# Kernel optimization log

Measured on AMD Instinct MI355X. Metric: run time of the kernel, lower is better.

The kernel has to match this reference:

```python
import jax, jax.numpy as jnp
import numpy as np

DIM = 768
HEADS = 12
HEAD_DIM = DIM // HEADS


def setup_inputs() -> dict:
    key = jax.random.key(0)
    ks = jax.random.split(key, 5)
    B, S = 4, 2048
    init = 0.02
    x = jax.random.normal(ks[0], (B, S, DIM), dtype=jnp.float32)
    w_qkv = jax.random.normal(ks[1], (DIM, 3 * DIM), dtype=jnp.float32) * init
    b_qkv = jnp.zeros((3 * DIM,), dtype=jnp.float32)
    w_out = jax.random.normal(ks[2], (DIM, DIM), dtype=jnp.float32) * init
    b_out = jnp.zeros((DIM,), dtype=jnp.float32)
    return {"x": x, "w_qkv": w_qkv, "b_qkv": b_qkv, "w_out": w_out, "b_out": b_out}


def reference(x, w_qkv, b_qkv, w_out, b_out):
    B, S, D = x.shape
    # QKV projection: [B,S,3D] -> [3,B,H,S,hd]
    qkv = x @ w_qkv + b_qkv
    qkv = qkv.reshape(B, S, 3, HEADS, HEAD_DIM).transpose(2, 0, 3, 1, 4)
    q, k, v = qkv[0], qkv[1], qkv[2]
    # NOTE: original scales by 1/sqrt(head_num), not 1/sqrt(head_dim)
    scale = 1.0 / jnp.sqrt(jnp.float32(HEADS))
    scores = jnp.einsum("bhqd,bhkd->bhqk", q, k) * scale
    attn = jax.nn.softmax(scores, axis=-1)
    out = jnp.einsum("bhqk,bhkd->bhqd", attn, v)
    out = out.transpose(0, 2, 1, 3).reshape(B, S, D)
    return out @ w_out + b_out
```

## Files before the change

### kernel.cpp

```cpp
#include <hip/hip_runtime.h>
#include <hip/hip_bf16.h>
#include <cstdint>
#include <cstddef>

#define HEADS 12
#define HD    64
#define NB    4
#define SEQ   2048
#define DIM   768
#define NQKV  2304

static constexpr float QSCALE = 0.2886751345948129f * 1.4426950408889634f;

typedef __attribute__((ext_vector_type(8))) short short8;
typedef __attribute__((ext_vector_type(4))) short short4v;
typedef __attribute__((ext_vector_type(4))) float f32x4;

__device__ inline unsigned short f2bf(float x) {
    union { float f; uint32_t u; } v; v.f = x;
    return (unsigned short)((v.u + 0x7fffu + ((v.u >> 16) & 1u)) >> 16);
}

__device__ inline unsigned short f2bf_fast(float x) {
    __hip_bfloat16 h = __float2bfloat16(x);
    unsigned short u;
    __builtin_memcpy(&u, &h, 2);
    return u;
}

__device__ inline void gld16(const void* g, void* l) {
    __builtin_amdgcn_global_load_lds(
        (const __attribute__((address_space(1))) unsigned int*)g,
        (__attribute__((address_space(3))) unsigned int*)l, 16, 0, 0);
}

__device__ inline void transpose_tile(
    const float* __restrict__ w, unsigned short* __restrict__ wT,
    int ncols, int nrows, int bx, int by, float (*tile)[65])
{
    const int k0 = by * 64;
    const int n0 = bx * 64;
    const int tr = threadIdx.x >> 4;
    const int tc4 = (threadIdx.x & 15) * 4;
    #pragma unroll
    for (int it = 0; it < 4; ++it) {
        const int kk = tr + it * 16;
        *reinterpret_cast<float4*>(&tile[kk][tc4]) =
            *reinterpret_cast<const float4*>(w + (size_t)(k0 + kk) * ncols + n0 + tc4);
    }
    __syncthreads();
    #pragma unroll
    for (int it = 0; it < 4; ++it) {
        const int nn = tr + it * 16;
        short4v o;
        #pragma unroll
        for (int r = 0; r < 4; ++r) o[r] = (short)f2bf(tile[tc4 + r][nn]);
        *reinterpret_cast<short4v*>(wT + (size_t)(n0 + nn) * nrows + k0 + tc4) = o;
    }
}

__global__ __launch_bounds__(256) void prep_kernel(
    const float* __restrict__ x, unsigned short* __restrict__ xb,
    const float* __restrict__ wq, unsigned short* __restrict__ wqT,
    const float* __restrict__ wo, unsigned short* __restrict__ woT)
{
    __shared__ float tile[64][65];
    const int bid = blockIdx.x;
    if (bid < 3072) {
        const size_t i = ((size_t)bid * 256 + threadIdx.x) * 8;
        const float4 a = *reinterpret_cast<const float4*>(x + i);
        const float4 b = *reinterpret_cast<const float4*>(x + i + 4);
        short8 o;
        o[0] = (short)f2bf(a.x); o[1] = (short)f2bf(a.y);
        o[2] = (short)f2bf(a.z); o[3] = (short)f2bf(a.w);
        o[4] = (short)f2bf(b.x); o[5] = (short)f2bf(b.y);
        o[6] = (short)f2bf(b.z); o[7] = (short)f2bf(b.w);
        *reinterpret_cast<short8*>(xb + i) = o;
    } else if (bid < 3072 + 432) {
        const int r = bid - 3072;
        transpose_tile(wq, wqT, NQKV, DIM, r % 36, r / 36, tile);
    } else {
        const int r = bid - 3504;
        transpose_tile(wo, woT, DIM, DIM, r % 12, r / 12, tile);
    }
}

__global__ __launch_bounds__(512) void qkv_gemm_bf16(
    const unsigned short* __restrict__ A,
    const unsigned short* __restrict__ BT,
    const float* __restrict__ bias,
    unsigned short* __restrict__ qb, unsigned short* __restrict__ kb,
    unsigned short* __restrict__ vt)
{
    __shared__ __align__(16) unsigned short As[2][128][64];
    __shared__ __align__(16) unsigned short Bs[2][128][64];

    const int tid = threadIdx.x;
    const int wave = tid >> 6;
    const int lane = tid & 63;
    const int col = lane & 15;
    const int g = lane >> 4;
    const int m0 = blockIdx.y * 128;
    const int n0 = blockIdx.x * 128;
    const int wr = wave >> 2;
    const int wc = wave & 3;

    f32x4 acc[4][2] = {};

    auto STAGE = [&](int kt, int bsel) {
        #pragma unroll
        for (int it = 0; it < 2; ++it) {
            const int slot = tid + it * 512;
            const int row = slot >> 3;
            const int cg = (slot & 7) ^ (row & 7);
            gld16(A + (size_t)(m0 + row) * DIM + kt + cg * 8,
                  &As[bsel][0][0] + (size_t)slot * 8);
            gld16(BT + (size_t)(n0 + row) * DIM + kt + cg * 8,
                  &Bs[bsel][0][0] + (size_t)slot * 8);
        }
    };

    const int NKT = DIM / 64;
    STAGE(0, 0);
    asm volatile("s_waitcnt vmcnt(0)" ::: "memory");
    __builtin_amdgcn_s_barrier();

    for (int t = 0; t < NKT; ++t) {
        const int cur = t & 1;
        if (t + 1 < NKT) STAGE((t + 1) * 64, cur ^ 1);

        #pragma unroll
        for (int ks = 0; ks < 2; ++ks) {
            short8 af[4], bf[2];
            #pragma unroll
            for (int i = 0; i < 4; ++i) {
                const int ra = wr * 64 + i * 16 + col;
                af[i] = *reinterpret_cast<const short8*>(
                    &As[cur][ra][(((ks * 4 + g) ^ (ra & 7)) << 3)]);
            }
            #pragma unroll
            for (int j = 0; j < 2; ++j) {
                const int rb = wc * 32 + j * 16 + col;
                bf[j] = *reinterpret_cast<const short8*>(
                    &Bs[cur][rb][(((ks * 4 + g) ^ (rb & 7)) << 3)]);
            }
            #pragma unroll
            for (int i = 0; i < 4; ++i)
                #pragma unroll
                for (int j = 0; j < 2; ++j)
                    acc[i][j] = __builtin_amdgcn_mfma_f32_16x16x32_bf16(
                        af[i], bf[j], acc[i][j], 0, 0, 0);
        }

        if (t + 1 < NKT) {
            asm volatile("s_waitcnt vmcnt(0)" ::: "memory");
            __builtin_amdgcn_s_barrier();
        }
    }

    const int which = n0 / DIM;
    #pragma unroll
    for (int j = 0; j < 2; ++j) {
        const int n = n0 + wc * 32 + j * 16 + col;
        const int rem = n - which * DIM;
        const int h = rem >> 6, dh = rem & 63;
        const float bj = bias[n];
        #pragma unroll
        for (int i = 0; i < 4; ++i) {
            const int mbase = m0 + wr * 64 + i * 16 + g * 4;
            const int b_ = mbase >> 11;
            const int s_ = mbase & 2047;
            const size_t bh = (size_t)(b_ * HEADS + h);
            if (which == 2) {
                short4v pk;
                #pragma unroll
                for (int r = 0; r < 4; ++r)
                    pk[r] = (short)f2bf(acc[i][j][r] + bj);
                *reinterpret_cast<short4v*>(vt + (bh * HD + dh) * SEQ + s_) = pk;
            } else {
                unsigned short* dst = (which == 0) ? qb : kb;
                const float sc = (which == 0) ? QSCALE : 1.0f;
                #pragma unroll
                for (int r = 0; r < 4; ++r)
                    dst[(bh * SEQ + s_ + r) * HD + dh] =
                        f2bf((acc[i][j][r] + bj) * sc);
            }
        }
    }
}

__global__ __launch_bounds__(512) void attn_kernel(
    const unsigned short* __restrict__ qb, const unsigned short* __restrict__ kbuf,
    const unsigned short* __restrict__ vt, unsigned short* __restrict__ ctxb)
{
    __shared__ __align__(16) unsigned short Ks[2][64][64];
    __shared__ __align__(16) unsigned short Vs[2][64][64];
    __shared__ __align__(16) unsigned short Ps[8][16][64];

    const int tid = threadIdx.x;
    const int wave = tid >> 6;
    const int lane = tid & 63;
    const int col = lane & 15;
    const int g   = lane >> 4;

    const int bid = blockIdx.x;
    const int vbid = (bid & 7) * 96 + (bid >> 3);
    const int bh = vbid >> 4;
    const int q0 = (vbid & 15) * 128;
    const int wq = q0 + wave * 16 + col;

    const size_t hb = (size_t)bh * SEQ * HD;

    short8 qf[2];
    {
        const unsigned short* src = qb + hb + (size_t)wq * HD + g * 8;
        qf[0] = *reinterpret_cast<const short8*>(src);
        qf[1] = *reinterpret_cast<const short8*>(src + 32);
    }

    const short ONE = (short)0x3F80;
    const short8 ONES = {ONE, ONE, ONE, ONE, ONE, ONE, ONE, ONE};

    f32x4 acc4[4] = {};
    f32x4 acc5 = {};

    const unsigned short* Kg = kbuf + hb;
    const unsigned short* Vg = vt + hb;

    const int srow = tid >> 3;
    const int scl  = tid & 7;
    const int scg  = scl ^ (srow & 7);

    auto STAGE = [&](int jt, int bsel) {
        const int kb0 = jt * 64;
        gld16(Kg + (size_t)(kb0 + srow) * HD + scg * 8,
              &Ks[bsel][0][0] + (size_t)tid * 8);
        gld16(Vg + (size_t)srow * SEQ + kb0 + scg * 8,
              &Vs[bsel][0][0] + (size_t)tid * 8);
    };

    const int NT = SEQ / 64;
    STAGE(0, 0);

    for (int jt = 0; jt < NT; ++jt) {
        const int cur = jt & 1;
        if (jt + 1 < NT) {
            STAGE(jt + 1, cur ^ 1);
            asm volatile("s_waitcnt vmcnt(2)" ::: "memory");
        } else {
            asm volatile("s_waitcnt vmcnt(0)" ::: "memory");
        }
        __builtin_amdgcn_s_barrier();

        f32x4 st[4] = {};
        __builtin_amdgcn_s_setprio(1);
        #pragma unroll
        for (int m = 0; m < 4; ++m) {
            const int row = m * 16 + col;
            const short8 kf0 = *reinterpret_cast<const short8*>(
                &Ks[cur][row][((g ^ (row & 7)) << 3)]);
            const short8 kf1 = *reinterpret_cast<const short8*>(
                &Ks[cur][row][(((g + 4) ^ (row & 7)) << 3)]);
            st[m] = __builtin_amdgcn_mfma_f32_16x16x32_bf16(kf0, qf[0], st[m], 0, 0, 0);
            st[m] = __builtin_amdgcn_mfma_f32_16x16x32_bf16(kf1, qf[1], st[m], 0, 0, 0);
        }
        __builtin_amdgcn_s_setprio(0);

        #pragma unroll
        for (int m = 0; m < 4; ++m) {
            float p[4];
            p[0] = __builtin_amdgcn_exp2f(st[m][0]);
            p[1] = __builtin_amdgcn_exp2f(st[m][1]);
            p[2] = __builtin_amdgcn_exp2f(st[m][2]);
            p[3] = __builtin_amdgcn_exp2f(st[m][3]);
            short4v pk;
            #pragma unroll
            for (int r = 0; r < 4; ++r) pk[r] = (short)f2bf_fast(p[r]);
            const int scw = (2 * m + (g >> 1)) ^ (col & 7);
            *reinterpret_cast<short4v*>(
                &Ps[wave][col][(scw << 3) + ((g & 1) << 2)]) = pk;
        }

        const short8 pf0 = *reinterpret_cast<const short8*>(
            &Ps[wave][col][((g ^ (col & 7)) << 3)]);
        const short8 pf1 = *reinterpret_cast<const short8*>(
            &Ps[wave][col][(((g + 4) ^ (col & 7)) << 3)]);

        __builtin_amdgcn_s_setprio(1);
        #pragma unroll
        for (int nb = 0; nb < 4; ++nb) {
            const int row = nb * 16 + col;
            const short8 vf0 = *reinterpret_cast<const short8*>(
                &Vs[cur][row][((g ^ (row & 7)) << 3)]);
            const short8 vf1 = *reinterpret_cast<const short8*>(
                &Vs[cur][row][(((g + 4) ^ (row & 7)) << 3)]);
            acc4[nb] = __builtin_amdgcn_mfma_f32_16x16x32_bf16(pf0, vf0, acc4[nb], 0, 0, 0);
            acc4[nb] = __builtin_amdgcn_mfma_f32_16x16x32_bf16(pf1, vf1, acc4[nb], 0, 0, 0);
        }
        acc5 = __builtin_amdgcn_mfma_f32_16x16x32_bf16(pf0, ONES, acc5, 0, 0, 0);
        acc5 = __builtin_amdgcn_mfma_f32_16x16x32_bf16(pf1, ONES, acc5, 0, 0, 0);
        __builtin_amdgcn_s_setprio(0);

        __builtin_amdgcn_s_barrier();
    }

    float lr[4];
    #pragma unroll
    for (int r = 0; r < 4; ++r) lr[r] = 1.0f / acc5[r];
    const int b_ = bh / HEADS;
    const int h = bh - b_ * HEADS;
    #pragma unroll
    for (int nb = 0; nb < 4; ++nb)
        #pragma unroll
        for (int r = 0; r < 4; ++r) {
            const int s_ = q0 + wave * 16 + g * 4 + r;
            ctxb[((size_t)b_ * SEQ + s_) * DIM + h * HD + nb * 16 + col] =
                f2bf_fast(acc4[nb][r] * lr[r]);
        }
}

__global__ __launch_bounds__(512) void out_gemm_bf16(
    const unsigned short* __restrict__ A,
    const unsigned short* __restrict__ BT,
    const float* __restrict__ bias, float* __restrict__ out)
{
    __shared__ __align__(16) unsigned short As[2][128][64];
    __shared__ __align__(16) unsigned short Bs[2][128][64];

    const int tid = threadIdx.x;
    const int wave = tid >> 6;
    const int lane = tid & 63;
    const int col = lane & 15;
    const int g = lane >> 4;
    const int m0 = blockIdx.y * 128;
    const int n0 = blockIdx.x * 128;
    const int wr = wave >> 2;
    const int wc = wave & 3;

    f32x4 acc[4][2] = {};

    auto STAGE = [&](int kt, int bsel) {
        #pragma unroll
        for (int it = 0; it < 2; ++it) {
            const int slot = tid + it * 512;
            const int row = slot >> 3;
            const int cg = (slot & 7) ^ (row & 7);
            gld16(A + (size_t)(m0 + row) * DIM + kt + cg * 8,
                  &As[bsel][0][0] + (size_t)slot * 8);
            gld16(BT + (size_t)(n0 + row) * DIM + kt + cg * 8,
                  &Bs[bsel][0][0] + (size_t)slot * 8);
        }
    };

    const int NKT = DIM / 64;
    STAGE(0, 0);
    asm volatile("s_waitcnt vmcnt(0)" ::: "memory");
    __builtin_amdgcn_s_barrier();

    for (int t = 0; t < NKT; ++t) {
        const int cur = t & 1;
        if (t + 1 < NKT) STAGE((t + 1) * 64, cur ^ 1);

        #pragma unroll
        for (int ks = 0; ks < 2; ++ks) {
            short8 af[4], bf[2];
            #pragma unroll
            for (int i = 0; i < 4; ++i) {
                const int ra = wr * 64 + i * 16 + col;
                af[i] = *reinterpret_cast<const short8*>(
                    &As[cur][ra][(((ks * 4 + g) ^ (ra & 7)) << 3)]);
            }
            #pragma unroll
            for (int j = 0; j < 2; ++j) {
                const int rb = wc * 32 + j * 16 + col;
                bf[j] = *reinterpret_cast<const short8*>(
                    &Bs[cur][rb][(((ks * 4 + g) ^ (rb & 7)) << 3)]);
            }
            #pragma unroll
            for (int i = 0; i < 4; ++i)
                #pragma unroll
                for (int j = 0; j < 2; ++j)
                    acc[i][j] = __builtin_amdgcn_mfma_f32_16x16x32_bf16(
                        af[i], bf[j], acc[i][j], 0, 0, 0);
        }

        if (t + 1 < NKT) {
            asm volatile("s_waitcnt vmcnt(0)" ::: "memory");
            __builtin_amdgcn_s_barrier();
        }
    }

    #pragma unroll
    for (int j = 0; j < 2; ++j) {
        const int n = n0 + wc * 32 + j * 16 + col;
        const float bj = bias[n];
        #pragma unroll
        for (int i = 0; i < 4; ++i) {
            const int m = m0 + wr * 64 + i * 16 + g * 4;
            #pragma unroll
            for (int r = 0; r < 4; ++r)
                out[(size_t)(m + r) * DIM + n] = acc[i][j][r] + bj;
        }
    }
}

extern "C" void kernel_launch(void* const* d_in, const int* in_sizes, int n_in,
                              void* d_out, int out_size, void* d_ws, size_t ws_size,
                              hipStream_t stream)
{
    const float* x     = (const float*)d_in[0];
    const float* w_qkv = (const float*)d_in[1];
    const float* b_qkv = (const float*)d_in[2];
    const float* w_out = (const float*)d_in[3];
    const float* b_out = (const float*)d_in[4];
    float* out = (float*)d_out;

    const size_t QSZ = (size_t)NB * HEADS * SEQ * HD;
    unsigned short* qb   = (unsigned short*)d_ws;
    unsigned short* kb   = qb + QSZ;
    unsigned short* vt   = kb + QSZ;
    unsigned short* xb   = vt + QSZ;
    unsigned short* ctxb = xb + QSZ;
    unsigned short* wqT  = ctxb + QSZ;
    unsigned short* woT  = wqT + (size_t)NQKV * DIM;

    prep_kernel<<<3648, 256, 0, stream>>>(x, xb, w_qkv, wqT, w_out, woT);
    qkv_gemm_bf16<<<dim3(NQKV / 128, (NB * SEQ) / 128), 512, 0, stream>>>(
        xb, wqT, b_qkv, qb, kb, vt);
    attn_kernel<<<dim3((SEQ / 128) * NB * HEADS), 512, 0, stream>>>(qb, kb, vt, ctxb);
    out_gemm_bf16<<<dim3(DIM / 128, (NB * SEQ) / 128), 512, 0, stream>>>(
        ctxb, woT, b_out, out);
}
```

Before: 147.9 us.

## Software-pipeline QK^T one tile ahead of softmax and PV in attention

Restructures the attention loop so the QK^T MFMAs for tile t run while exp2/PV for tile t-1 are processed, with V triple-buffered in shared memory to allow the skew. One barrier per iteration replaces two, and loads are issued after the barrier with a full vmcnt(0) wait. This aims to overlap the exp/convert work with matrix instructions, at the cost of extra LDS for the third V buffer and more live registers.

```diff
diff --git a/kernel.cpp b/kernel.cpp
--- a/kernel.cpp
+++ b/kernel.cpp
@@ -194,7 +194,7 @@
     const unsigned short* __restrict__ vt, unsigned short* __restrict__ ctxb)
 {
     __shared__ __align__(16) unsigned short Ks[2][64][64];
-    __shared__ __align__(16) unsigned short Vs[2][64][64];
+    __shared__ __align__(16) unsigned short Vs[3][64][64];
     __shared__ __align__(16) unsigned short Ps[8][16][64];
 
     const int tid = threadIdx.x;
@@ -231,48 +231,60 @@
     const int scl  = tid & 7;
     const int scg  = scl ^ (srow & 7);
 
-    auto STAGE = [&](int jt, int bsel) {
+    auto STAGE = [&](int jt, int kbsel, int vbsel) {
         const int kb0 = jt * 64;
         gld16(Kg + (size_t)(kb0 + srow) * HD + scg * 8,
-              &Ks[bsel][0][0] + (size_t)tid * 8);
+              &Ks[kbsel][0][0] + (size_t)tid * 8);
         gld16(Vg + (size_t)srow * SEQ + kb0 + scg * 8,
-              &Vs[bsel][0][0] + (size_t)tid * 8);
+              &Vs[vbsel][0][0] + (size_t)tid * 8);
     };
 
     const int NT = SEQ / 64;
-    STAGE(0, 0);
-
-    for (int jt = 0; jt < NT; ++jt) {
-        const int cur = jt & 1;
-        if (jt + 1 < NT) {
-            STAGE(jt + 1, cur ^ 1);
-            asm volatile("s_waitcnt vmcnt(2)" ::: "memory");
-        } else {
-            asm volatile("s_waitcnt vmcnt(0)" ::: "memory");
-        }
+
+    STAGE(0, 0, 0);
+    asm volatile("s_waitcnt vmcnt(0)" ::: "memory");
+    __builtin_amdgcn_s_barrier();
+    STAGE(1, 1, 1);
+
+    f32x4 stp[4] = {};
+    #pragma unroll
+    for (int m = 0; m < 4; ++m) {
+        const int row = m * 16 + col;
+        const short8 kf0 = *reinterpret_cast<const short8*>(
+            &Ks[0][row][((g ^ (row & 7)) << 3)]);
+        const short8 kf1 = *reinterpret_cast<const short8*>(
+            &Ks[0][row][(((g + 4) ^ (row & 7)) << 3)]);
+        stp[m] = __builtin_amdgcn_mfma_f32_16x16x32_bf16(kf0, qf[0], stp[m], 0, 0, 0);
+        stp[m] = __builtin_amdgcn_mfma_f32_16x16x32_bf16(kf1, qf[1], stp[m], 0, 0, 0);
+    }
+
+    int vm1 = 0, vcur = 1, vnxt = 2;
+
+    for (int t = 1; t < NT; ++t) {
+        const int kcur = t & 1;
+        asm volatile("s_waitcnt vmcnt(0)" ::: "memory");
         __builtin_amdgcn_s_barrier();
-
-        f32x4 st[4] = {};
-        __builtin_amdgcn_s_setprio(1);
+        if (t + 1 < NT) STAGE(t + 1, kcur ^ 1, vnxt);
+
+        f32x4 stn[4] = {};
         #pragma unroll
         for (int m = 0; m < 4; ++m) {
             const int row = m * 16 + col;
             const short8 kf0 = *reinterpret_cast<const short8*>(
-                &Ks[cur][row][((g ^ (row & 7)) << 3)]);
+                &Ks[kcur][row][((g ^ (row & 7)) << 3)]);
             const short8 kf1 = *reinterpret_cast<const short8*>(
-                &Ks[cur][row][(((g + 4) ^ (row & 7)) << 3)]);
-            st[m] = __builtin_amdgcn_mfma_f32_16x16x32_bf16(kf0, qf[0], st[m], 0, 0, 0);
-            st[m] = __builtin_amdgcn_mfma_f32_16x16x32_bf16(kf1, qf[1], st[m], 0, 0, 0);
-        }
-        __builtin_amdgcn_s_setprio(0);
+                &Ks[kcur][row][(((g + 4) ^ (row & 7)) << 3)]);
+            stn[m] = __builtin_amdgcn_mfma_f32_16x16x32_bf16(kf0, qf[0], stn[m], 0, 0, 0);
+            stn[m] = __builtin_amdgcn_mfma_f32_16x16x32_bf16(kf1, qf[1], stn[m], 0, 0, 0);
+        }
 
         #pragma unroll
         for (int m = 0; m < 4; ++m) {
             float p[4];
-            p[0] = __builtin_amdgcn_exp2f(st[m][0]);
-            p[1] = __builtin_amdgcn_exp2f(st[m][1]);
-            p[2] = __builtin_amdgcn_exp2f(st[m][2]);
-            p[3] = __builtin_amdgcn_exp2f(st[m][3]);
+            p[0] = __builtin_amdgcn_exp2f(stp[m][0]);
+            p[1] = __builtin_amdgcn_exp2f(stp[m][1]);
+            p[2] = __builtin_amdgcn_exp2f(stp[m][2]);
+            p[3] = __builtin_amdgcn_exp2f(stp[m][3]);
             short4v pk;
             #pragma unroll
             for (int r = 0; r < 4; ++r) pk[r] = (short)f2bf_fast(p[r]);
@@ -280,7 +292,6 @@
             *reinterpret_cast<short4v*>(
                 &Ps[wave][col][(scw << 3) + ((g & 1) << 2)]) = pk;
         }
-
         const short8 pf0 = *reinterpret_cast<const short8*>(
             &Ps[wave][col][((g ^ (col & 7)) << 3)]);
         const short8 pf1 = *reinterpret_cast<const short8*>(
@@ -291,9 +302,9 @@
         for (int nb = 0; nb < 4; ++nb) {
             const int row = nb * 16 + col;
             const short8 vf0 = *reinterpret_cast<const short8*>(
-                &Vs[cur][row][((g ^ (row & 7)) << 3)]);
+                &Vs[vm1][row][((g ^ (row & 7)) << 3)]);
             const short8 vf1 = *reinterpret_cast<const short8*>(
-                &Vs[cur][row][(((g + 4) ^ (row & 7)) << 3)]);
+                &Vs[vm1][row][(((g + 4) ^ (row & 7)) << 3)]);
             acc4[nb] = __builtin_amdgcn_mfma_f32_16x16x32_bf16(pf0, vf0, acc4[nb], 0, 0, 0);
             acc4[nb] = __builtin_amdgcn_mfma_f32_16x16x32_bf16(pf1, vf1, acc4[nb], 0, 0, 0);
         }
@@ -301,7 +312,42 @@
         acc5 = __builtin_amdgcn_mfma_f32_16x16x32_bf16(pf1, ONES, acc5, 0, 0, 0);
         __builtin_amdgcn_s_setprio(0);
 
-        __builtin_amdgcn_s_barrier();
+        #pragma unroll
+        for (int m = 0; m < 4; ++m) stp[m] = stn[m];
+        vm1 = vcur; vcur = vnxt; vnxt = (vnxt + 1 == 3) ? 0 : vnxt + 1;
+    }
+
+    {
+        #pragma unroll
+        for (int m = 0; m < 4; ++m) {
+            float p[4];
+            p[0] = __builtin_amdgcn_exp2f(stp[m][0]);
+            p[1] = __builtin_amdgcn_exp2f(stp[m][1]);
+            p[2] = __builtin_amdgcn_exp2f(stp[m][2]);
+            p[3] = __builtin_amdgcn_exp2f(stp[m][3]);
+            short4v pk;
+            #pragma unroll
+            for (int r = 0; r < 4; ++r) pk[r] = (short)f2bf_fast(p[r]);
+            const int scw = (2 * m + (g >> 1)) ^ (col & 7);
+            *reinterpret_cast<short4v*>(
+                &Ps[wave][col][(scw << 3) + ((g & 1) << 2)]) = pk;
+        }
+        const short8 pf0 = *reinterpret_cast<const short8*>(
+            &Ps[wave][col][((g ^ (col & 7)) << 3)]);
+        const short8 pf1 = *reinterpret_cast<const short8*>(
+            &Ps[wave][col][(((g + 4) ^ (col & 7)) << 3)]);
+        #pragma unroll
+        for (int nb = 0; nb < 4; ++nb) {
+            const int row = nb * 16 + col;
+            const short8 vf0 = *reinterpret_cast<const short8*>(
+                &Vs[vm1][row][((g ^ (row & 7)) << 3)]);
+            const short8 vf1 = *reinterpret_cast<const short8*>(
+                &Vs[vm1][row][(((g + 4) ^ (row & 7)) << 3)]);
+            acc4[nb] = __builtin_amdgcn_mfma_f32_16x16x32_bf16(pf0, vf0, acc4[nb], 0, 0, 0);
+            acc4[nb] = __builtin_amdgcn_mfma_f32_16x16x32_bf16(pf1, vf1, acc4[nb], 0, 0, 0);
+        }
+        acc5 = __builtin_amdgcn_mfma_f32_16x16x32_bf16(pf0, ONES, acc5, 0, 0, 0);
+        acc5 = __builtin_amdgcn_mfma_f32_16x16x32_bf16(pf1, ONES, acc5, 0, 0, 0);
     }
 
     float lr[4];
```

New measurement: 157.0 us. +6.1%, slower.

## Give each attention wave two query sub-tiles to reuse K/V fragments

Applied to the files above, without the earlier changes.

The attention kernel drops from 8 waves of 16 query rows each to 4 waves of 32 rows each (two 16-row sub-tiles), keeping the 128-query block. Each K and V fragment read from shared memory now feeds two MFMA chains, halving LDS reads per unit of MFMA work. Staging is split across two loads per thread and the wait count is adjusted to match. In exchange, register use per wave roughly doubles and there are fewer waves per block to hide latency.

```diff
diff --git a/kernel.cpp b/kernel.cpp
--- a/kernel.cpp
+++ b/kernel.cpp
@@ -189,13 +189,13 @@
     }
 }
 
-__global__ __launch_bounds__(512) void attn_kernel(
+__global__ __launch_bounds__(256) void attn_kernel(
     const unsigned short* __restrict__ qb, const unsigned short* __restrict__ kbuf,
     const unsigned short* __restrict__ vt, unsigned short* __restrict__ ctxb)
 {
     __shared__ __align__(16) unsigned short Ks[2][64][64];
     __shared__ __align__(16) unsigned short Vs[2][64][64];
-    __shared__ __align__(16) unsigned short Ps[8][16][64];
+    __shared__ __align__(16) unsigned short Ps[4][2][16][64];
 
     const int tid = threadIdx.x;
     const int wave = tid >> 6;
@@ -207,36 +207,41 @@
     const int vbid = (bid & 7) * 96 + (bid >> 3);
     const int bh = vbid >> 4;
     const int q0 = (vbid & 15) * 128;
-    const int wq = q0 + wave * 16 + col;
 
     const size_t hb = (size_t)bh * SEQ * HD;
 
-    short8 qf[2];
-    {
-        const unsigned short* src = qb + hb + (size_t)wq * HD + g * 8;
-        qf[0] = *reinterpret_cast<const short8*>(src);
-        qf[1] = *reinterpret_cast<const short8*>(src + 32);
+    short8 qf[2][2];
+    #pragma unroll
+    for (int qs = 0; qs < 2; ++qs) {
+        const unsigned short* src =
+            qb + hb + (size_t)(q0 + wave * 32 + qs * 16 + col) * HD + g * 8;
+        qf[qs][0] = *reinterpret_cast<const short8*>(src);
+        qf[qs][1] = *reinterpret_cast<const short8*>(src + 32);
     }
 
     const short ONE = (short)0x3F80;
     const short8 ONES = {ONE, ONE, ONE, ONE, ONE, ONE, ONE, ONE};
 
-    f32x4 acc4[4] = {};
-    f32x4 acc5 = {};
+    f32x4 acc4[2][4] = {};
+    f32x4 acc5[2] = {};
 
     const unsigned short* Kg = kbuf + hb;
     const unsigned short* Vg = vt + hb;
 
     const int srow = tid >> 3;
     const int scl  = tid & 7;
-    const int scg  = scl ^ (srow & 7);
 
     auto STAGE = [&](int jt, int bsel) {
         const int kb0 = jt * 64;
-        gld16(Kg + (size_t)(kb0 + srow) * HD + scg * 8,
-              &Ks[bsel][0][0] + (size_t)tid * 8);
-        gld16(Vg + (size_t)srow * SEQ + kb0 + scg * 8,
-              &Vs[bsel][0][0] + (size_t)tid * 8);
+        #pragma unroll
+        for (int it = 0; it < 2; ++it) {
+            const int row = srow + it * 32;
+            const int cg = scl ^ (row & 7);
+            gld16(Kg + (size_t)(kb0 + row) * HD + cg * 8,
+                  &Ks[bsel][0][0] + (size_t)(it * 256 + tid) * 8);
+            gld16(Vg + (size_t)row * SEQ + kb0 + cg * 8,
+                  &Vs[bsel][0][0] + (size_t)(it * 256 + tid) * 8);
+        }
     };
 
     const int NT = SEQ / 64;
@@ -246,13 +251,13 @@
         const int cur = jt & 1;
         if (jt + 1 < NT) {
             STAGE(jt + 1, cur ^ 1);
-            asm volatile("s_waitcnt vmcnt(2)" ::: "memory");
+            asm volatile("s_waitcnt vmcnt(4)" ::: "memory");
         } else {
             asm volatile("s_waitcnt vmcnt(0)" ::: "memory");
         }
         __builtin_amdgcn_s_barrier();
 
-        f32x4 st[4] = {};
+        f32x4 st[2][4] = {};
         __builtin_amdgcn_s_setprio(1);
         #pragma unroll
         for (int m = 0; m < 4; ++m) {
@@ -261,30 +266,42 @@
                 &Ks[cur][row][((g ^ (row & 7)) << 3)]);
             const short8 kf1 = *reinterpret_cast<const short8*>(
                 &Ks[cur][row][(((g + 4) ^ (row & 7)) << 3)]);
-            st[m] = __builtin_amdgcn_mfma_f32_16x16x32_bf16(kf0, qf[0], st[m], 0, 0, 0);
-            st[m] = __builtin_amdgcn_mfma_f32_16x16x32_bf16(kf1, qf[1], st[m], 0, 0, 0);
+            #pragma unroll
+            for (int qs = 0; qs < 2; ++qs) {
+                st[qs][m] = __builtin_amdgcn_mfma_f32_16x16x32_bf16(
+                    kf0, qf[qs][0], st[qs][m], 0, 0, 0);
+                st[qs][m] = __builtin_amdgcn_mfma_f32_16x16x32_bf16(
+                    kf1, qf[qs][1], st[qs][m], 0, 0, 0);
+            }
         }
         __builtin_amdgcn_s_setprio(0);
 
         #pragma unroll
-        for (int m = 0; m < 4; ++m) {
-            float p[4];
-            p[0] = __builtin_amdgcn_exp2f(st[m][0]);
-            p[1] = __builtin_amdgcn_exp2f(st[m][1]);
-            p[2] = __builtin_amdgcn_exp2f(st[m][2]);
-            p[3] = __builtin_amdgcn_exp2f(st[m][3]);
-            short4v pk;
-            #pragma unroll
-            for (int r = 0; r < 4; ++r) pk[r] = (short)f2bf_fast(p[r]);
-            const int scw = (2 * m + (g >> 1)) ^ (col & 7);
-            *reinterpret_cast<short4v*>(
-                &Ps[wave][col][(scw << 3) + ((g & 1) << 2)]) = pk;
-        }
-
-        const short8 pf0 = *reinterpret_cast<const short8*>(
-            &Ps[wave][col][((g ^ (col & 7)) << 3)]);
-        const short8 pf1 = *reinterpret_cast<const short8*>(
-            &Ps[wave][col][(((g + 4) ^ (col & 7)) << 3)]);
+        for (int qs = 0; qs < 2; ++qs) {
+            #pragma unroll
+            for (int m = 0; m < 4; ++m) {
+                float p[4];
+                p[0] = __builtin_amdgcn_exp2f(st[qs][m][0]);
+                p[1] = __builtin_amdgcn_exp2f(st[qs][m][1]);
+                p[2] = __builtin_amdgcn_exp2f(st[qs][m][2]);
+                p[3] = __builtin_amdgcn_exp2f(st[qs][m][3]);
+                short4v pk;
+                #pragma unroll
+                for (int r = 0; r < 4; ++r) pk[r] = (short)f2bf_fast(p[r]);
+                const int scw = (2 * m + (g >> 1)) ^ (col & 7);
+                *reinterpret_cast<short4v*>(
+                    &Ps[wave][qs][col][(scw << 3) + ((g & 1) << 2)]) = pk;
+            }
+        }
+
+        short8 pf[2][2];
+        #pragma unroll
+        for (int qs = 0; qs < 2; ++qs) {
+            pf[qs][0] = *reinterpret_cast<const short8*>(
+                &Ps[wave][qs][col][((g ^ (col & 7)) << 3)]);
+            pf[qs][1] = *reinterpret_cast<const short8*>(
+                &Ps[wave][qs][col][(((g + 4) ^ (col & 7)) << 3)]);
+        }
 
         __builtin_amdgcn_s_setprio(1);
         #pragma unroll
@@ -294,29 +311,42 @@
                 &Vs[cur][row][((g ^ (row & 7)) << 3)]);
             const short8 vf1 = *reinterpret_cast<const short8*>(
                 &Vs[cur][row][(((g + 4) ^ (row & 7)) << 3)]);
-            acc4[nb] = __builtin_amdgcn_mfma_f32_16x16x32_bf16(pf0, vf0, acc4[nb], 0, 0, 0);
-            acc4[nb] = __builtin_amdgcn_mfma_f32_16x16x32_bf16(pf1, vf1, acc4[nb], 0, 0, 0);
-        }
-        acc5 = __builtin_amdgcn_mfma_f32_16x16x32_bf16(pf0, ONES, acc5, 0, 0, 0);
-        acc5 = __builtin_amdgcn_mfma_f32_16x16x32_bf16(pf1, ONES, acc5, 0, 0, 0);
+            #pragma unroll
+            for (int qs = 0; qs < 2; ++qs) {
+                acc4[qs][nb] = __builtin_amdgcn_mfma_f32_16x16x32_bf16(
+                    pf[qs][0], vf0, acc4[qs][nb], 0, 0, 0);
+                acc4[qs][nb] = __builtin_amdgcn_mfma_f32_16x16x32_bf16(
+                    pf[qs][1], vf1, acc4[qs][nb], 0, 0, 0);
+            }
+        }
+        #pragma unroll
+        for (int qs = 0; qs < 2; ++qs) {
+            acc5[qs] = __builtin_amdgcn_mfma_f32_16x16x32_bf16(
+                pf[qs][0], ONES, acc5[qs], 0, 0, 0);
+            acc5[qs] = __builtin_amdgcn_mfma_f32_16x16x32_bf16(
+                pf[qs][1], ONES, acc5[qs], 0, 0, 0);
+        }
         __builtin_amdgcn_s_setprio(0);
 
         __builtin_amdgcn_s_barrier();
     }
 
-    float lr[4];
-    #pragma unroll
-    for (int r = 0; r < 4; ++r) lr[r] = 1.0f / acc5[r];
     const int b_ = bh / HEADS;
     const int h = bh - b_ * HEADS;
     #pragma unroll
-    for (int nb = 0; nb < 4; ++nb)
-        #pragma unroll
-        for (int r = 0; r < 4; ++r) {
-            const int s_ = q0 + wave * 16 + g * 4 + r;
-            ctxb[((size_t)b_ * SEQ + s_) * DIM + h * HD + nb * 16 + col] =
-                f2bf_fast(acc4[nb][r] * lr[r]);
-        }
+    for (int qs = 0; qs < 2; ++qs) {
+        float lr[4];
+        #pragma unroll
+        for (int r = 0; r < 4; ++r) lr[r] = 1.0f / acc5[qs][r];
+        #pragma unroll
+        for (int nb = 0; nb < 4; ++nb)
+            #pragma unroll
+            for (int r = 0; r < 4; ++r) {
+                const int s_ = q0 + wave * 32 + qs * 16 + g * 4 + r;
+                ctxb[((size_t)b_ * SEQ + s_) * DIM + h * HD + nb * 16 + col] =
+                    f2bf_fast(acc4[qs][nb][r] * lr[r]);
+            }
+    }
 }
 
 __global__ __launch_bounds__(512) void out_gemm_bf16(
@@ -427,7 +457,7 @@
     prep_kernel<<<3648, 256, 0, stream>>>(x, xb, w_qkv, wqT, w_out, woT);
     qkv_gemm_bf16<<<dim3(NQKV / 128, (NB * SEQ) / 128), 512, 0, stream>>>(
         xb, wqT, b_qkv, qb, kb, vt);
-    attn_kernel<<<dim3((SEQ / 128) * NB * HEADS), 512, 0, stream>>>(qb, kb, vt, ctxb);
+    attn_kernel<<<dim3((SEQ / 128) * NB * HEADS), 256, 0, stream>>>(qb, kb, vt, ctxb);
     out_gemm_bf16<<<dim3(DIM / 128, (NB * SEQ) / 128), 512, 0, stream>>>(
         ctxb, woT, b_out, out);
 }
```

Result: slower. 175.7 us (+18.8%).
